# Optimization experiments

Hardware: AMD Instinct MI355X
Metric: run time of the kernel (lower is better)

Reference implementation:

```python
import jax, jax.numpy as jnp
import numpy as np

# dims
B, S, LC, K, CE, L, WE, H = 64, 512, 16, 3, 10, 32, 200, 200
V, A, T = 50000, 128, 64
LP = LC + K - 1  # padded word length (pad_word adds (K-1)/2 on each side)
D_IN = WE + L    # LSTM input dim = 232


def setup_inputs() -> dict:
    key = jax.random.key(0)
    ks = jax.random.split(key, 16)
    f = lambda k, shp: jax.random.normal(k, shp, dtype=jnp.float32) * 0.05
    return {
        "char_ids": jax.random.randint(ks[0], (B, S, LP), 0, A),
        "word_ids": jax.random.randint(ks[1], (B, S), 0, V),
        "word_emb": f(ks[2], (V, WE)),
        "char_emb": f(ks[3], (A, CE)),
        "conv_w": f(ks[4], (L, K * CE)),   # Conv1d(1, l, K*CE) == linear 30->32
        "conv_b": f(ks[5], (L,)),
        "w_ih_f": f(ks[6], (4 * H, D_IN)),
        "w_hh_f": f(ks[7], (4 * H, H)),
        "b_ih_f": f(ks[8], (4 * H,)),
        "b_hh_f": f(ks[9], (4 * H,)),
        "w_ih_b": f(ks[10], (4 * H, D_IN)),
        "w_hh_b": f(ks[11], (4 * H, H)),
        "b_ih_b": f(ks[12], (4 * H,)),
        "b_hh_b": f(ks[13], (4 * H,)),
        "out_w": f(ks[14], (T, 2 * H)),
        "out_b": f(ks[15], (T,)),
    }


def _lstm(x, w_ih, w_hh, b_ih, b_hh, reverse):
    # x: [S, B, D]; PyTorch gate order i, f, g, o
    def step(carry, x_t):
        h, c = carry
        g = x_t @ w_ih.T + b_ih + h @ w_hh.T + b_hh
        i, f, gg, o = jnp.split(g, 4, axis=-1)
        c = jax.nn.sigmoid(f) * c + jax.nn.sigmoid(i) * jnp.tanh(gg)
        h = jax.nn.sigmoid(o) * jnp.tanh(c)
        return (h, c), h

    b = x.shape[1]
    init = (jnp.zeros((b, H), x.dtype), jnp.zeros((b, H), x.dtype))
    _, hs = jax.lax.scan(step, init, x, reverse=reverse)
    return hs  # [S, B, H]


def reference(char_ids, word_ids, word_emb, char_emb, conv_w, conv_b,
              w_ih_f, w_hh_f, b_ih_f, b_hh_f,
              w_ih_b, w_hh_b, b_ih_b, b_hh_b,
              out_w, out_b):
    # per-word char CNN + max-pool, fully batched over (B, S, windows)
    ce = char_emb[char_ids]                                    # [B,S,LP,CE]
    # sliding K-char windows, flattened to K*CE (== original x_hat construction)
    win = jnp.concatenate([ce[:, :, k:k + LC] for k in range(K)], axis=-1)  # [B,S,LC,K*CE]
    phi = jnp.einsum('bswd,ld->bswl', win, conv_w) + conv_b    # tiny conv == linear
    char_repr = phi.max(axis=2)                                # max-pool over positions -> [B,S,L]

    combined = jnp.concatenate([word_emb[word_ids], char_repr], axis=-1)  # [B,S,232]
    x = combined.reshape(S, B, D_IN)  # faithful to original .view (reshape, not transpose)

    hf = _lstm(x, w_ih_f, w_hh_f, b_ih_f, b_hh_f, reverse=False)
    hb = _lstm(x, w_ih_b, w_hh_b, b_ih_b, b_hh_b, reverse=True)
    lstm_out = jnp.concatenate([hf, hb], axis=-1)              # [S,B,2H]  (dropout: eval mode)

    tag_space = lstm_out.reshape(B, S, 2 * H) @ out_w.T + out_b  # faithful .view back
    return jax.nn.log_softmax(tag_space, axis=1)  # original normalizes over dim=1 (seq axis)
```

## Files before the change

kernel.cpp:

```cpp
#include <hip/hip_runtime.h>
#include <hip/hip_bf16.h>
#include <math.h>

constexpr int B_ = 64, S_ = 512, LP_ = 18, CE_ = 10, LF_ = 32;
constexpr int WE_ = 200, H_ = 200, T_ = 64;
constexpr int N_ = B_ * S_;
constexpr int KP_ = 256;
constexpr int G4_ = 800;
constexpr int NG_ = 1600;

typedef short short8 __attribute__((ext_vector_type(8)));
typedef float f32x4 __attribute__((ext_vector_type(4)));

__device__ __forceinline__ ushort bf16bits(float v) {
  return __bfloat16_as_ushort(__float2bfloat16(v));
}
__device__ __forceinline__ float bf2f(ushort u) {
  return __uint_as_float(((uint)u) << 16);
}
__device__ __forceinline__ float sigf(float x) {
  return __builtin_amdgcn_rcpf(1.f + __expf(-x));
}
__device__ __forceinline__ float tanhfast(float x) {
  return 2.f * __builtin_amdgcn_rcpf(1.f + __expf(-2.f * x)) - 1.f;
}

__global__ __launch_bounds__(256) void k_build_x(
    const int* __restrict__ char_ids, const int* __restrict__ word_ids,
    const float* __restrict__ word_emb, const float* __restrict__ char_emb,
    const float* __restrict__ conv_w, const float* __restrict__ conv_b,
    ushort* __restrict__ Xb)
{
  __shared__ float ce[4][LP_ * CE_];
  const int wave = threadIdx.x >> 6, lane = threadIdx.x & 63;
  const int n = blockIdx.x * 4 + wave;

  for (int i = lane; i < LP_ * CE_; i += 64) {
    int c = char_ids[n * LP_ + i / CE_];
    ce[wave][i] = char_emb[c * CE_ + (i % CE_)];
  }
  const float* we = word_emb + (size_t)word_ids[n] * WE_;
  ushort* xr = Xb + (size_t)n * KP_;
  for (int i = lane; i < WE_; i += 64) xr[i] = bf16bits(we[i]);
  if (lane < KP_ - WE_ - LF_) xr[WE_ + LF_ + lane] = 0;
  __syncthreads();

  const int f = lane & 31, half = lane >> 5;
  float cw[30];
  #pragma unroll
  for (int i = 0; i < 30; ++i) cw[i] = conv_w[f * 30 + i];
  float m = -1e30f;
  for (int w = half * 8; w < half * 8 + 8; ++w) {
    float acc = 0.f;
    #pragma unroll
    for (int i = 0; i < 30; ++i) acc += ce[wave][w * CE_ + i] * cw[i];
    m = fmaxf(m, acc);
  }
  m = fmaxf(m, __shfl_xor(m, 32));
  if (half == 0) xr[WE_ + f] = bf16bits(m + conv_b[f]);
}

__global__ __launch_bounds__(64) void k_pack_w(
    const float* __restrict__ w_ih_f, const float* __restrict__ w_ih_b,
    const float* __restrict__ b_ih_f, const float* __restrict__ b_hh_f,
    const float* __restrict__ b_ih_b, const float* __restrict__ b_hh_b,
    ushort* __restrict__ Wb, float* __restrict__ biasc)
{
  const int r = blockIdx.x;
  const float* src = r < G4_ ? w_ih_f + (size_t)r * 232 : w_ih_b + (size_t)(r - G4_) * 232;
  for (int c = threadIdx.x; c < KP_; c += 64)
    Wb[(size_t)r * KP_ + c] = (c < 232) ? bf16bits(src[c]) : (ushort)0;
  if (threadIdx.x == 0)
    biasc[r] = r < G4_ ? (b_ih_f[r] + b_hh_f[r]) : (b_ih_b[r - G4_] + b_hh_b[r - G4_]);
}

__global__ __launch_bounds__(256) void k_gemm_proj(
    const ushort* __restrict__ Xb, const ushort* __restrict__ Wb,
    const float* __restrict__ biasc, ushort* __restrict__ Gc)
{
  __shared__ __align__(16) char smem[65536];
  const int tid = threadIdx.x;
  const int lane = tid & 63, w = tid >> 6;
  const int wr = w >> 1, wc = w & 1;
  const int rowbase = blockIdx.y * 64, colbase = blockIdx.x * 64;

  const char* Ag = (const char*)(Xb + (size_t)rowbase * KP_);
  const char* Bg = (const char*)(Wb + (size_t)colbase * KP_);
  #pragma unroll
  for (int it = 0; it < 8; ++it) {
    int slot = it * 256 + tid;
    int row = slot >> 5, c16 = slot & 31;
    int src = row * 512 + c16 * 16;
    int dst = row * 512 + ((c16 * 16) ^ ((row & 7) << 4));
    *(short8*)(smem + dst) = *(const short8*)(Ag + src);
    *(short8*)(smem + 32768 + dst) = *(const short8*)(Bg + src);
  }
  __syncthreads();

  f32x4 acc[2][2] = {};
  #pragma unroll
  for (int kk = 0; kk < 8; ++kk) {
    const int kb = kk * 64 + (lane >> 4) * 16;
    short8 a[2], b[2];
    #pragma unroll
    for (int m = 0; m < 2; ++m) {
      int ar = wr * 32 + m * 16 + (lane & 15);
      a[m] = *(const short8*)(smem + ar * 512 + (kb ^ ((ar & 7) << 4)));
      int bc = wc * 32 + m * 16 + (lane & 15);
      b[m] = *(const short8*)(smem + 32768 + bc * 512 + (kb ^ ((bc & 7) << 4)));
    }
    #pragma unroll
    for (int m = 0; m < 2; ++m)
      #pragma unroll
      for (int n = 0; n < 2; ++n)
        acc[m][n] = __builtin_amdgcn_mfma_f32_16x16x32_bf16(a[m], b[n], acc[m][n], 0, 0, 0);
  }
  __syncthreads();

  float* Cs = (float*)smem;
  #pragma unroll
  for (int m = 0; m < 2; ++m)
    #pragma unroll
    for (int n = 0; n < 2; ++n)
      #pragma unroll
      for (int i = 0; i < 4; ++i) {
        int r = wr * 32 + m * 16 + (lane >> 4) * 4 + i;
        int c = wc * 32 + n * 16 + (lane & 15);
        Cs[r * 65 + c] = acc[m][n][i];
      }
  __syncthreads();

  const int r = tid >> 2, cg = (tid & 3) * 16;
  ushort ob[16];
  #pragma unroll
  for (int j = 0; j < 16; ++j)
    ob[j] = bf16bits(Cs[r * 65 + cg + j] + biasc[colbase + cg + j]);
  ushort* dst = Gc + (size_t)(rowbase + r) * NG_ + colbase + cg;
  *(short8*)(dst) = *(short8*)(ob);
  *(short8*)(dst + 8) = *(short8*)(ob + 8);
}

__global__ __launch_bounds__(512, 2) void k_lstm(
    const ushort* __restrict__ Gc,
    const float* __restrict__ w_hh_f, const float* __restrict__ w_hh_b,
    ushort* __restrict__ hf, ushort* __restrict__ hb)
{
  __shared__ ushort h_lds[2][16][232];
  __shared__ __align__(16) char wlds45[2][65536];
  __shared__ __align__(16) char wlds6[16384];

  const int tid = threadIdx.x;
  const int lane = tid & 63, w = tid >> 6;
  const int lo = lane & 15, hi = lane >> 4;
  const int dir = blockIdx.x >> 3, grp = blockIdx.x & 7;
  const float* Whh = dir ? w_hh_b : w_hh_f;
  ushort* hout = dir ? hb : hf;
  const bool real_chain = lo < 8;

  for (int i = tid; i < 2 * 16 * 232; i += 512) ((ushort*)h_lds)[i] = 0;

  const int s0 = 2 * w, s1 = 2 * w + 1;
  const int off0 = s0 < 12 ? 12 * s0 : 144 + 16 * (s0 - 12);
  const int off1 = s1 < 12 ? 12 * s1 : 144 + 16 * (s1 - 12);
  const int cnt0 = s0 < 12 ? 12 : 16;
  const int cnt1 = s1 < 12 ? 12 : 16;
  const int rl0 = min(cnt0, 200 - off0);
  const int rl1 = min(cnt1, 200 - off1);
  const int offs[2] = {off0, off1};
  const int rls[2]  = {rl0, rl1};

  short8 wreg[2][4][4];
  #pragma unroll
  for (int sl = 0; sl < 2; ++sl) {
    const int off = offs[sl], rl = rls[sl];
    const bool rowok = lo < rl;
    const int s = 2 * w + sl;
    #pragma unroll
    for (int g = 0; g < 4; ++g) {
      const float* wr = Whh + (size_t)(g * 200 + off + lo) * 200;
      const int gid = s * 4 + g;
      #pragma unroll
      for (int kt = 0; kt < 7; ++kt) {
        const int k0 = kt * 32 + hi * 8;
        float v[8];
        if (rowok && k0 < 200) {
          float4 p0 = *(const float4*)(wr + k0);
          float4 p1 = *(const float4*)(wr + k0 + 4);
          v[0] = p0.x; v[1] = p0.y; v[2] = p0.z; v[3] = p0.w;
          v[4] = p1.x; v[5] = p1.y; v[6] = p1.z; v[7] = p1.w;
        } else {
          #pragma unroll
          for (int j = 0; j < 8; ++j) v[j] = 0.f;
        }
        short8 fr;
        #pragma unroll
        for (int j = 0; j < 8; ++j) fr[j] = (short)bf16bits(v[j]);
        if (kt < 4) wreg[sl][g][kt] = fr;
        else if (kt < 6) *(short8*)(wlds45[kt - 4] + gid * 1024 + lane * 16) = fr;
        else if (hi == 0) *(short8*)(wlds6 + gid * 256 + lo * 16) = fr;
      }
    }
  }

  float c_[2][4] = {};

  const int rowsel = real_chain ? lo : 0;
  const int step0 = dir ? (S_ - 1) : 0;
  const ushort* gp = Gc + (size_t)(step0 * 64 + grp * 8 + rowsel) * NG_ + dir * G4_ + hi * 4;
  ushort* hp = hout + (size_t)(step0 * 64 + grp * 8 + lo) * H_ + hi * 4;
  const ptrdiff_t gstep = (dir ? -64 : 64) * (ptrdiff_t)NG_;
  const ptrdiff_t hstep = (dir ? -64 : 64) * (ptrdiff_t)H_;

  uint2 preA[2][4], preB[2][4];
  #pragma unroll
  for (int sl = 0; sl < 2; ++sl)
    #pragma unroll
    for (int g = 0; g < 4; ++g)
      preA[sl][g] = *(const uint2*)(gp + g * 200 + offs[sl]);
  gp += gstep;

  __syncthreads();

  auto lstm_step = [&](const ushort (*HR)[232], ushort (*HW)[232],
                       uint2 (&pc)[2][4], uint2 (&pn)[2][4]) {
    #pragma unroll
    for (int sl = 0; sl < 2; ++sl)
      #pragma unroll
      for (int g = 0; g < 4; ++g)
        pn[sl][g] = *(const uint2*)(gp + g * 200 + offs[sl]);

    f32x4 acc[2][4] = {};
    const char* hrow = (const char*)HR + lo * 464 + hi * 16;
    #pragma unroll
    for (int kt = 0; kt < 7; ++kt) {
      short8 hfr = *(const short8*)(hrow + kt * 64);
      if (kt < 4) {
        #pragma unroll
        for (int sl = 0; sl < 2; ++sl)
          #pragma unroll
          for (int g = 0; g < 4; ++g)
            acc[sl][g] = __builtin_amdgcn_mfma_f32_16x16x32_bf16(
                wreg[sl][g][kt], hfr, acc[sl][g], 0, 0, 0);
      } else if (kt < 6) {
        #pragma unroll
        for (int sl = 0; sl < 2; ++sl)
          #pragma unroll
          for (int g = 0; g < 4; ++g) {
            const int gid = (2 * w + sl) * 4 + g;
            short8 wk = *(const short8*)(wlds45[kt - 4] + gid * 1024 + lane * 16);
            acc[sl][g] = __builtin_amdgcn_mfma_f32_16x16x32_bf16(wk, hfr, acc[sl][g], 0, 0, 0);
          }
      } else {
        #pragma unroll
        for (int sl = 0; sl < 2; ++sl)
          #pragma unroll
          for (int g = 0; g < 4; ++g) {
            const int gid = (2 * w + sl) * 4 + g;
            short8 wk = {};
            if (hi == 0) wk = *(const short8*)(wlds6 + gid * 256 + lo * 16);
            acc[sl][g] = __builtin_amdgcn_mfma_f32_16x16x32_bf16(wk, hfr, acc[sl][g], 0, 0, 0);
          }
      }
    }

    char* hwr = (char*)HW + lo * 464 + hi * 8;
    #pragma unroll
    for (int sl = 0; sl < 2; ++sl) {
      const int rl = rls[sl];
      float hv[4];
      #pragma unroll
      for (int i = 0; i < 4; ++i) {
        const uint2 pi = pc[sl][0], pf = pc[sl][1], pg = pc[sl][2], po = pc[sl][3];
        const uint wi = (i < 2) ? pi.x : pi.y;
        const uint wf = (i < 2) ? pf.x : pf.y;
        const uint wg = (i < 2) ? pg.x : pg.y;
        const uint wo = (i < 2) ? po.x : po.y;
        const int sh = (i & 1) * 16;
        float gi = acc[sl][0][i] + bf2f((ushort)(wi >> sh));
        float gf = acc[sl][1][i] + bf2f((ushort)(wf >> sh));
        float gg = acc[sl][2][i] + bf2f((ushort)(wg >> sh));
        float go = acc[sl][3][i] + bf2f((ushort)(wo >> sh));
        float cn = sigf(gf) * c_[sl][i] + sigf(gi) * tanhfast(gg);
        c_[sl][i] = cn;
        hv[i] = sigf(go) * tanhfast(cn);
      }
      if (real_chain && hi * 4 < rl) {
        uint2 pk;
        pk.x = (uint)bf16bits(hv[0]) | ((uint)bf16bits(hv[1]) << 16);
        pk.y = (uint)bf16bits(hv[2]) | ((uint)bf16bits(hv[3]) << 16);
        *(uint2*)(hp + offs[sl]) = pk;
        *(uint2*)(hwr + offs[sl] * 2) = pk;
      }
    }

    __syncthreads();
    gp += gstep;
    hp += hstep;
  };

  for (int tt = 0; tt < S_; tt += 2) {
    lstm_step(h_lds[0], h_lds[1], preA, preB);
    lstm_step(h_lds[1], h_lds[0], preB, preA);
  }
}

__global__ __launch_bounds__(256) void k_out(
    const ushort* __restrict__ hf, const ushort* __restrict__ hb,
    const float* __restrict__ out_w, const float* __restrict__ out_b,
    float* __restrict__ tag)
{
  const int m = threadIdx.x >> 3;
  const int tg = threadIdx.x & 7;
  const int n = blockIdx.x * 32 + m;
  const ushort* hfp = hf + (size_t)n * H_;
  const ushort* hbp = hb + (size_t)n * H_;
  float acc[8];
  #pragma unroll
  for (int q = 0; q < 8; ++q) acc[q] = out_b[tg + 8 * q];
  for (int k = 0; k < H_ / 4; ++k) {
    uint2 hv = *(const uint2*)(hfp + k * 4);
    float x0 = bf2f((ushort)hv.x), x1 = bf2f((ushort)(hv.x >> 16));
    float x2 = bf2f((ushort)hv.y), x3 = bf2f((ushort)(hv.y >> 16));
    #pragma unroll
    for (int q = 0; q < 8; ++q) {
      float4 w = ((const float4*)(out_w + (size_t)(tg + 8 * q) * 2 * H_))[k];
      acc[q] += x0 * w.x + x1 * w.y + x2 * w.z + x3 * w.w;
    }
  }
  for (int k = 0; k < H_ / 4; ++k) {
    uint2 hv = *(const uint2*)(hbp + k * 4);
    float x0 = bf2f((ushort)hv.x), x1 = bf2f((ushort)(hv.x >> 16));
    float x2 = bf2f((ushort)hv.y), x3 = bf2f((ushort)(hv.y >> 16));
    #pragma unroll
    for (int q = 0; q < 8; ++q) {
      float4 w = ((const float4*)(out_w + (size_t)(tg + 8 * q) * 2 * H_ + H_))[k];
      acc[q] += x0 * w.x + x1 * w.y + x2 * w.z + x3 * w.w;
    }
  }
  #pragma unroll
  for (int q = 0; q < 8; ++q) tag[(size_t)n * T_ + tg + 8 * q] = acc[q];
}

__global__ __launch_bounds__(256) void k_lsm(
    const float* __restrict__ tag, float* __restrict__ out)
{
  __shared__ float red[4][T_];
  __shared__ float lse[T_];
  const int b = blockIdx.x;
  const int tt = threadIdx.x & 63, ch = threadIdx.x >> 6;
  const float* tb = tag + (size_t)b * S_ * T_;

  float m = -1e30f;
  for (int s = ch * 128; s < ch * 128 + 128; ++s) m = fmaxf(m, tb[s * T_ + tt]);
  red[ch][tt] = m;
  __syncthreads();
  if (ch == 0)
    lse[tt] = fmaxf(fmaxf(red[0][tt], red[1][tt]), fmaxf(red[2][tt], red[3][tt]));
  __syncthreads();
  m = lse[tt];
  float sum = 0.f;
  for (int s = ch * 128; s < ch * 128 + 128; ++s) sum += __expf(tb[s * T_ + tt] - m);
  __syncthreads();
  red[ch][tt] = sum;
  __syncthreads();
  if (ch == 0)
    lse[tt] = m + logf(red[0][tt] + red[1][tt] + red[2][tt] + red[3][tt]);
  __syncthreads();
  const float l = lse[tt];
  float* ob = out + (size_t)b * S_ * T_;
  for (int s = ch * 128; s < ch * 128 + 128; ++s) ob[s * T_ + tt] = tb[s * T_ + tt] - l;
}

extern "C" void kernel_launch(void* const* d_in, const int* in_sizes, int n_in,
                              void* d_out, int out_size, void* d_ws, size_t ws_size,
                              hipStream_t stream) {
  const int*   char_ids = (const int*)d_in[0];
  const int*   word_ids = (const int*)d_in[1];
  const float* word_emb = (const float*)d_in[2];
  const float* char_emb = (const float*)d_in[3];
  const float* conv_w   = (const float*)d_in[4];
  const float* conv_b   = (const float*)d_in[5];
  const float* w_ih_f   = (const float*)d_in[6];
  const float* w_hh_f   = (const float*)d_in[7];
  const float* b_ih_f   = (const float*)d_in[8];
  const float* b_hh_f   = (const float*)d_in[9];
  const float* w_ih_b   = (const float*)d_in[10];
  const float* w_hh_b   = (const float*)d_in[11];
  const float* b_ih_b   = (const float*)d_in[12];
  const float* b_hh_b   = (const float*)d_in[13];
  const float* out_w    = (const float*)d_in[14];
  const float* out_b    = (const float*)d_in[15];

  char* ws = (char*)d_ws;
  ushort* Xb    = (ushort*)(ws);
  ushort* Wb    = (ushort*)(ws + 16777216);
  float*  biasc = (float*) (ws + 17596416);
  ushort* Gc    = (ushort*)(ws + 18422016);
  ushort* hf    = (ushort*)(ws + 123279616);
  ushort* hb    = (ushort*)(ws + 136386816);
  float*  tag   = (float*) (ws + 149494016);

  hipLaunchKernelGGL(k_build_x, dim3(N_ / 4), dim3(256), 0, stream,
                     char_ids, word_ids, word_emb, char_emb, conv_w, conv_b, Xb);
  hipLaunchKernelGGL(k_pack_w, dim3(NG_), dim3(64), 0, stream,
                     w_ih_f, w_ih_b, b_ih_f, b_hh_f, b_ih_b, b_hh_b, Wb, biasc);
  hipLaunchKernelGGL(k_gemm_proj, dim3(NG_ / 64, N_ / 64), dim3(256), 0, stream,
                     Xb, Wb, biasc, Gc);
  hipLaunchKernelGGL(k_lstm, dim3(16), dim3(512), 0, stream, Gc, w_hh_f, w_hh_b, hf, hb);
  hipLaunchKernelGGL(k_out, dim3(N_ / 32), dim3(256), 0, stream, hf, hb, out_w, out_b, tag);
  hipLaunchKernelGGL(k_lsm, dim3(B_), dim3(256), 0, stream, tag, (float*)d_out);
}
```

Measured before the change: 1.621 ms.

## Fold log2e scaling into LSTM weights and keep more W_hh tiles in registers

Prescales the input-projection and recurrent weights and biases by log2(e), doubled for the g gate, so gate activations use a raw v_exp_f32 (exp2) without a multiply. It moves the kt=4 recurrent weight tile from LDS into registers, drops the two-blocks-per-CU launch bound, and adds a zero pad region in LDS so the kt=6 load needs no branch. It also removes the one-step-ahead prefetch of Gc in favour of loading within each step, and raises wave priority around the MFMA section. The aim is to shorten the serial per-step latency of the recurrence. The cost is higher register pressure, and the projection loads are no longer hidden behind the previous step.

```diff
diff --git a/kernel.cpp b/kernel.cpp
--- a/kernel.cpp
+++ b/kernel.cpp
@@ -8,6 +8,7 @@
 constexpr int KP_ = 256;
 constexpr int G4_ = 800;
 constexpr int NG_ = 1600;
+constexpr float L2E_ = 1.4426950408889634f;
 
 typedef short short8 __attribute__((ext_vector_type(8)));
 typedef float f32x4 __attribute__((ext_vector_type(4)));
@@ -18,11 +19,11 @@
 __device__ __forceinline__ float bf2f(ushort u) {
   return __uint_as_float(((uint)u) << 16);
 }
-__device__ __forceinline__ float sigf(float x) {
-  return __builtin_amdgcn_rcpf(1.f + __expf(-x));
-}
-__device__ __forceinline__ float tanhfast(float x) {
-  return 2.f * __builtin_amdgcn_rcpf(1.f + __expf(-2.f * x)) - 1.f;
+__device__ __forceinline__ float exp2fast(float x) {
+  float r; asm("v_exp_f32 %0, %1" : "=v"(r) : "v"(x)); return r;
+}
+__device__ __forceinline__ float sig2(float y) {
+  return __builtin_amdgcn_rcpf(1.f + exp2fast(-y));
 }
 
 __global__ __launch_bounds__(256) void k_build_x(
@@ -67,11 +68,14 @@
     ushort* __restrict__ Wb, float* __restrict__ biasc)
 {
   const int r = blockIdx.x;
-  const float* src = r < G4_ ? w_ih_f + (size_t)r * 232 : w_ih_b + (size_t)(r - G4_) * 232;
+  const int rl = r < G4_ ? r : r - G4_;
+  const int gate = rl / 200;
+  const float sc = (gate == 2) ? 2.f * L2E_ : L2E_;
+  const float* src = r < G4_ ? w_ih_f + (size_t)rl * 232 : w_ih_b + (size_t)rl * 232;
   for (int c = threadIdx.x; c < KP_; c += 64)
-    Wb[(size_t)r * KP_ + c] = (c < 232) ? bf16bits(src[c]) : (ushort)0;
+    Wb[(size_t)r * KP_ + c] = (c < 232) ? bf16bits(src[c] * sc) : (ushort)0;
   if (threadIdx.x == 0)
-    biasc[r] = r < G4_ ? (b_ih_f[r] + b_hh_f[r]) : (b_ih_b[r - G4_] + b_hh_b[r - G4_]);
+    biasc[r] = sc * (r < G4_ ? (b_ih_f[rl] + b_hh_f[rl]) : (b_ih_b[rl] + b_hh_b[rl]));
 }
 
 __global__ __launch_bounds__(256) void k_gemm_proj(
@@ -140,14 +144,14 @@
   *(short8*)(dst + 8) = *(short8*)(ob + 8);
 }
 
-__global__ __launch_bounds__(512, 2) void k_lstm(
+__global__ __launch_bounds__(512) void k_lstm(
     const ushort* __restrict__ Gc,
     const float* __restrict__ w_hh_f, const float* __restrict__ w_hh_b,
     ushort* __restrict__ hf, ushort* __restrict__ hb)
 {
   __shared__ ushort h_lds[2][16][232];
-  __shared__ __align__(16) char wlds45[2][65536];
-  __shared__ __align__(16) char wlds6[16384];
+  __shared__ __align__(16) char wlds5[65536];
+  __shared__ __align__(16) char wlds6[17408];
 
   const int tid = threadIdx.x;
   const int lane = tid & 63, w = tid >> 6;
@@ -155,21 +159,19 @@
   const int dir = blockIdx.x >> 3, grp = blockIdx.x & 7;
   const float* Whh = dir ? w_hh_b : w_hh_f;
   ushort* hout = dir ? hb : hf;
-  const bool real_chain = lo < 8;
 
   for (int i = tid; i < 2 * 16 * 232; i += 512) ((ushort*)h_lds)[i] = 0;
+  if (tid < 256) ((uint*)(wlds6 + 16384))[tid] = 0;
 
   const int s0 = 2 * w, s1 = 2 * w + 1;
   const int off0 = s0 < 12 ? 12 * s0 : 144 + 16 * (s0 - 12);
   const int off1 = s1 < 12 ? 12 * s1 : 144 + 16 * (s1 - 12);
-  const int cnt0 = s0 < 12 ? 12 : 16;
-  const int cnt1 = s1 < 12 ? 12 : 16;
-  const int rl0 = min(cnt0, 200 - off0);
-  const int rl1 = min(cnt1, 200 - off1);
+  const int rl0 = min(s0 < 12 ? 12 : 16, 200 - off0);
+  const int rl1 = min(s1 < 12 ? 12 : 16, 200 - off1);
   const int offs[2] = {off0, off1};
   const int rls[2]  = {rl0, rl1};
 
-  short8 wreg[2][4][4];
+  short8 wreg[2][4][5];
   #pragma unroll
   for (int sl = 0; sl < 2; ++sl) {
     const int off = offs[sl], rl = rls[sl];
@@ -177,6 +179,7 @@
     const int s = 2 * w + sl;
     #pragma unroll
     for (int g = 0; g < 4; ++g) {
+      const float sc = (g == 2) ? 2.f * L2E_ : L2E_;
       const float* wr = Whh + (size_t)(g * 200 + off + lo) * 200;
       const int gid = s * 4 + g;
       #pragma unroll
@@ -194,9 +197,9 @@
         }
         short8 fr;
         #pragma unroll
-        for (int j = 0; j < 8; ++j) fr[j] = (short)bf16bits(v[j]);
-        if (kt < 4) wreg[sl][g][kt] = fr;
-        else if (kt < 6) *(short8*)(wlds45[kt - 4] + gid * 1024 + lane * 16) = fr;
+        for (int j = 0; j < 8; ++j) fr[j] = (short)bf16bits(v[j] * sc);
+        if (kt < 5) wreg[sl][g][kt] = fr;
+        else if (kt == 5) *(short8*)(wlds5 + gid * 1024 + lane * 16) = fr;
         else if (hi == 0) *(short8*)(wlds6 + gid * 256 + lo * 16) = fr;
       }
     }
@@ -204,50 +207,47 @@
 
   float c_[2][4] = {};
 
-  const int rowsel = real_chain ? lo : 0;
+  const int rowsel = lo & 7;
   const int step0 = dir ? (S_ - 1) : 0;
-  const ushort* gp = Gc + (size_t)(step0 * 64 + grp * 8 + rowsel) * NG_ + dir * G4_ + hi * 4;
+  const ushort* gpp = Gc + (size_t)(step0 * 64 + grp * 8 + rowsel) * NG_ + dir * G4_ + hi * 4;
   ushort* hp = hout + (size_t)(step0 * 64 + grp * 8 + lo) * H_ + hi * 4;
   const ptrdiff_t gstep = (dir ? -64 : 64) * (ptrdiff_t)NG_;
   const ptrdiff_t hstep = (dir ? -64 : 64) * (ptrdiff_t)H_;
 
-  uint2 preA[2][4], preB[2][4];
+  int b6o[2];
   #pragma unroll
   for (int sl = 0; sl < 2; ++sl)
-    #pragma unroll
-    for (int g = 0; g < 4; ++g)
-      preA[sl][g] = *(const uint2*)(gp + g * 200 + offs[sl]);
-  gp += gstep;
-
-  __syncthreads();
-
-  auto lstm_step = [&](const ushort (*HR)[232], ushort (*HW)[232],
-                       uint2 (&pc)[2][4], uint2 (&pn)[2][4]) {
+    b6o[sl] = (hi == 0) ? ((2 * w + sl) * 4 * 256 + lo * 16) : (16384 + lo * 16);
+
+  __syncthreads();
+
+  auto lstm_step = [&](const ushort (*HR)[232], ushort (*HW)[232]) {
+    uint2 pre[2][4];
     #pragma unroll
     for (int sl = 0; sl < 2; ++sl)
       #pragma unroll
       for (int g = 0; g < 4; ++g)
-        pn[sl][g] = *(const uint2*)(gp + g * 200 + offs[sl]);
-
+        pre[sl][g] = *(const uint2*)(gpp + g * 200 + offs[sl]);
+
+    __builtin_amdgcn_s_setprio(1);
     f32x4 acc[2][4] = {};
     const char* hrow = (const char*)HR + lo * 464 + hi * 16;
     #pragma unroll
     for (int kt = 0; kt < 7; ++kt) {
       short8 hfr = *(const short8*)(hrow + kt * 64);
-      if (kt < 4) {
+      if (kt < 5) {
         #pragma unroll
         for (int sl = 0; sl < 2; ++sl)
           #pragma unroll
           for (int g = 0; g < 4; ++g)
             acc[sl][g] = __builtin_amdgcn_mfma_f32_16x16x32_bf16(
                 wreg[sl][g][kt], hfr, acc[sl][g], 0, 0, 0);
-      } else if (kt < 6) {
+      } else if (kt == 5) {
         #pragma unroll
         for (int sl = 0; sl < 2; ++sl)
           #pragma unroll
           for (int g = 0; g < 4; ++g) {
-            const int gid = (2 * w + sl) * 4 + g;
-            short8 wk = *(const short8*)(wlds45[kt - 4] + gid * 1024 + lane * 16);
+            short8 wk = *(const short8*)(wlds5 + ((2 * w + sl) * 4 + g) * 1024 + lane * 16);
             acc[sl][g] = __builtin_amdgcn_mfma_f32_16x16x32_bf16(wk, hfr, acc[sl][g], 0, 0, 0);
           }
       } else {
@@ -255,22 +255,19 @@
         for (int sl = 0; sl < 2; ++sl)
           #pragma unroll
           for (int g = 0; g < 4; ++g) {
-            const int gid = (2 * w + sl) * 4 + g;
-            short8 wk = {};
-            if (hi == 0) wk = *(const short8*)(wlds6 + gid * 256 + lo * 16);
+            short8 wk = *(const short8*)(wlds6 + b6o[sl] + g * 256);
             acc[sl][g] = __builtin_amdgcn_mfma_f32_16x16x32_bf16(wk, hfr, acc[sl][g], 0, 0, 0);
           }
       }
     }
-
-    char* hwr = (char*)HW + lo * 464 + hi * 8;
+    __builtin_amdgcn_s_setprio(0);
+
     #pragma unroll
     for (int sl = 0; sl < 2; ++sl) {
-      const int rl = rls[sl];
+      const uint2 pi = pre[sl][0], pf = pre[sl][1], pg = pre[sl][2], po = pre[sl][3];
       float hv[4];
       #pragma unroll
       for (int i = 0; i < 4; ++i) {
-        const uint2 pi = pc[sl][0], pf = pc[sl][1], pg = pc[sl][2], po = pc[sl][3];
         const uint wi = (i < 2) ? pi.x : pi.y;
         const uint wf = (i < 2) ? pf.x : pf.y;
         const uint wg = (i < 2) ? pg.x : pg.y;
@@ -280,27 +277,32 @@
         float gf = acc[sl][1][i] + bf2f((ushort)(wf >> sh));
         float gg = acc[sl][2][i] + bf2f((ushort)(wg >> sh));
         float go = acc[sl][3][i] + bf2f((ushort)(wo >> sh));
-        float cn = sigf(gf) * c_[sl][i] + sigf(gi) * tanhfast(gg);
+        float si = sig2(gi);
+        float sf = sig2(gf);
+        float so = sig2(go);
+        float tg = 2.f * sig2(gg) - 1.f;
+        float cn = sf * c_[sl][i] + si * tg;
         c_[sl][i] = cn;
-        hv[i] = sigf(go) * tanhfast(cn);
+        float tc = 2.f * sig2(cn * (2.f * L2E_)) - 1.f;
+        hv[i] = so * tc;
       }
-      if (real_chain && hi * 4 < rl) {
+      if (lo < 8 && hi * 4 < rls[sl]) {
         uint2 pk;
         pk.x = (uint)bf16bits(hv[0]) | ((uint)bf16bits(hv[1]) << 16);
         pk.y = (uint)bf16bits(hv[2]) | ((uint)bf16bits(hv[3]) << 16);
         *(uint2*)(hp + offs[sl]) = pk;
-        *(uint2*)(hwr + offs[sl] * 2) = pk;
+        *(uint2*)((char*)HW + lo * 464 + offs[sl] * 2 + hi * 8) = pk;
       }
     }
 
     __syncthreads();
-    gp += gstep;
+    gpp += gstep;
     hp += hstep;
   };
 
   for (int tt = 0; tt < S_; tt += 2) {
-    lstm_step(h_lds[0], h_lds[1], preA, preB);
-    lstm_step(h_lds[1], h_lds[0], preB, preA);
+    lstm_step(h_lds[0], h_lds[1]);
+    lstm_step(h_lds[1], h_lds[0]);
   }
 }
 
```

Result: slower. 2.581 ms (+59.3%).
